# Optimization experiments

Hardware: AMD Instinct MI355X
Metric: run time of the kernel (lower is better)

Reference implementation:

```python
import jax, jax.numpy as jnp
import numpy as np

FILTER_SIZE = (9, 9)
N_ITER = 5  # training-mode iteration count (module forces 5 in train, 10 in eval)
DN = ('NCHW', 'OIHW', 'NCHW')


def _gauss_kernel1d(inv_theta, spacing, fsize):
    half = fsize // 2
    d = spacing * jnp.arange(-half, half + 1, dtype=jnp.float32)
    k = jnp.exp(-(d * inv_theta) ** 2 / 2)
    # zero out the center tap (message passing excludes self)
    return k * (jnp.arange(fsize) != half).astype(k.dtype)


def _blur_single(x, spacing, inv_theta):
    # x: (C, H, W); separable gaussian filtering with 'same' output via pre-padding
    ph, pw = FILTER_SIZE[0] // 2, FILTER_SIZE[1] // 2
    xp = jnp.pad(x, ((0, 0), (ph, ph), (pw, pw)))[:, None]  # (C, 1, H+2ph, W+2pw)
    kh = _gauss_kernel1d(inv_theta[0], spacing[0], FILTER_SIZE[0])
    kw = _gauss_kernel1d(inv_theta[1], spacing[1], FILTER_SIZE[1])
    xp = jax.lax.conv_general_dilated(xp, kh[None, None, :, None], (1, 1), 'VALID', dimension_numbers=DN)
    xp = jax.lax.conv_general_dilated(xp, kw[None, None, None, :], (1, 1), 'VALID', dimension_numbers=DN)
    return xp[:, 0]  # (C, H, W)


def setup_inputs() -> dict:
    key = jax.random.key(0)
    k1, _ = jax.random.split(key)
    B, H, W, C = 16, 384, 384, 21
    x = jax.random.normal(k1, (B, H, W, C), dtype=jnp.float32)
    spatial_spacings = jnp.ones((B, 2), dtype=jnp.float32)
    smoothness_weight = jnp.asarray(1.0, dtype=jnp.float32)
    inv_smoothness_theta = jnp.full((2,), 1.0 / 0.5, dtype=jnp.float32)  # 1/theta
    return {
        'x': x,
        'spatial_spacings': spatial_spacings,
        'smoothness_weight': smoothness_weight,
        'inv_smoothness_theta': inv_smoothness_theta,
    }


def reference(x, spatial_spacings, smoothness_weight, inv_smoothness_theta):
    xt = jnp.transpose(x, (0, 3, 1, 2))  # (B, C, H, W)
    negative_unary = xt
    C = xt.shape[1]
    # compatibility: -(l1 == l2) -> -I_C
    compat = -jnp.eye(C, dtype=xt.dtype)
    blur = jax.vmap(_blur_single, in_axes=(0, 0, None))

    def body(xc, _):
        p = jax.nn.softmax(xc, axis=1)
        s = smoothness_weight * blur(p, spatial_spacings, inv_smoothness_theta)
        c = jnp.einsum('bjhw,jk->bkhw', s, compat)
        return negative_unary - c, None

    xt, _ = jax.lax.scan(body, xt, None, length=N_ITER)
    # returns == 'logits'
    return jnp.transpose(xt, (0, 2, 3, 1))
```

## Files before the change

kernel.cpp:

```cpp
#include <hip/hip_runtime.h>
#include <hip/hip_fp16.h>


#define BB    16
#define Himg  384
#define Wimg  384
#define CC    21
#define TH    16
#define TW    16
#define RR    4
#define PH    (TH + 2*RR)
#define PW    (TW + 2*RR)
#define ROWF  (PW * CC)
#define NPIX  (PH * PW)
#define OUT_ELEMS (TH * TW * CC)
#define CHUNKS_ROW (ROWF / 4)
#define NCHUNK (PH * CHUNKS_ROW)
#define NTOT  (BB * Himg * Wimg * CC)

__global__ __launch_bounds__(256, 6)
void crf_iter_kernel(const float* __restrict__ xin,
                     const float* __restrict__ unary,
                     float* __restrict__ out,
                     const float* __restrict__ spacings,
                     const float* __restrict__ inv_theta,
                     const float* __restrict__ sw_ptr)
{
    __shared__ __align__(16) unsigned char smem[PH * ROWF * 2];
    __half* pbuf = (__half*)smem;

    const int tid = threadIdx.x;
    const int b   = blockIdx.z;
    const int h0  = blockIdx.y * TH;
    const int w0  = blockIdx.x * TW;

    const float sp_h = spacings[b * 2 + 0];
    const float sp_w = spacings[b * 2 + 1];
    const float ith  = inv_theta[0];
    const float itw  = inv_theta[1];
    const float sw   = sw_ptr[0];
    float kh[9], kw[9];
#pragma unroll
    for (int i = 0; i < 9; ++i) {
        float dh = sp_h * (float)(i - 4) * ith;
        float dw = sp_w * (float)(i - 4) * itw;
        kh[i] = (i == 4) ? 0.f : __expf(-0.5f * dh * dh);
        kw[i] = (i == 4) ? 0.f : __expf(-0.5f * dw * dw);
    }

    {
        uint2* pb8 = (uint2*)pbuf;
        for (int idx = tid; idx < NCHUNK; idx += 256) {
            int r  = idx / CHUNKS_ROW;
            int q  = idx - r * CHUNKS_ROW;
            int hh = h0 - RR + r;
            if (hh >= 0 && hh < Himg) {
                int basef = ((b * Himg + hh) * Wimg + (w0 - RR)) * CC + q * 4;
                int a = basef < 0 ? 0 : (basef > NTOT - 4 ? NTOT - 4 : basef);
                float4 v = *(const float4*)(xin + a);
                __half2 lo = __floats2half2_rn(v.x, v.y);
                __half2 hi = __floats2half2_rn(v.z, v.w);
                uint2 st;
                st.x = *(unsigned int*)&lo;
                st.y = *(unsigned int*)&hi;
                pb8[idx] = st;
            }
        }
    }
    __syncthreads();

    for (int p = tid; p < NPIX; p += 256) {
        int r   = p / PW;
        int cpx = p - r * PW;
        int hh  = h0 - RR + r;
        int gw  = w0 - RR + cpx;
        __half* px = pbuf + p * CC;
        if (hh >= 0 && hh < Himg && gw >= 0 && gw < Wimg) {
            float v[CC];
            float m = -1e30f;
#pragma unroll
            for (int c = 0; c < CC; ++c) { v[c] = __half2float(px[c]); m = fmaxf(m, v[c]); }
            float s = 0.f;
#pragma unroll
            for (int c = 0; c < CC; ++c) { v[c] = __expf(v[c] - m); s += v[c]; }
            float inv = 1.f / s;
#pragma unroll
            for (int c = 0; c < CC; ++c) px[c] = __float2half_rn(v[c] * inv);
        } else {
            const __half z = __float2half_rn(0.f);
#pragma unroll
            for (int c = 0; c < CC; ++c) px[c] = z;
        }
    }
    __syncthreads();

    if (tid < ROWF / 2) {
        __half2* pb2 = (__half2*)pbuf;
        const int o2 = tid;
        float2 v[PH];
#pragma unroll
        for (int r = 0; r < PH; ++r) v[r] = __half22float2(pb2[r * (ROWF / 2) + o2]);
#pragma unroll
        for (int t = 0; t < TH; ++t) {
            float ax = 0.f, ay = 0.f;
#pragma unroll
            for (int i = 0; i < 9; ++i) {
                if (i == 4) continue;
                ax = fmaf(kh[i], v[t + i].x, ax);
                ay = fmaf(kh[i], v[t + i].y, ay);
            }
            __half2 o; o.x = __float2half_rn(ax); o.y = __float2half_rn(ay);
            pb2[t * (ROWF / 2) + o2] = o;
        }
    }
    __syncthreads();

    for (int o = tid; o < TH * CC; o += 256) {
        int h = o / CC;
        int c = o - h * CC;
        __half* line = pbuf + h * ROWF + c;
        float v[PW];
#pragma unroll
        for (int wp = 0; wp < PW; ++wp) v[wp] = __half2float(line[wp * CC]);
#pragma unroll
        for (int wt = 0; wt < TW; ++wt) {
            float acc = 0.f;
#pragma unroll
            for (int j = 0; j < 9; ++j) {
                if (j == 4) continue;
                acc = fmaf(kw[j], v[wt + j], acc);
            }
            line[wt * CC] = __float2half_rn(sw * acc);
        }
    }
    __syncthreads();

    {
        const int gbase = ((b * Himg + h0) * Wimg + w0) * CC;
        for (int j = tid; j < OUT_ELEMS / 4; j += 256) {
            int hrow = j / (TW * CC / 4);
            int qq   = j - hrow * (TW * CC / 4);
            int g = gbase + hrow * (Wimg * CC) + qq * 4;
            float4 u = *(const float4*)(unary + g);
            const __half2* sh = (const __half2*)(pbuf + hrow * ROWF + qq * 4);
            float2 lo = __half22float2(sh[0]);
            float2 hi = __half22float2(sh[1]);
            float4 o;
            o.x = u.x + lo.x; o.y = u.y + lo.y;
            o.z = u.z + hi.x; o.w = u.w + hi.y;
            *(float4*)(out + g) = o;
        }
    }
}

extern "C" void kernel_launch(void* const* d_in, const int* in_sizes, int n_in,
                              void* d_out, int out_size, void* d_ws, size_t ws_size,
                              hipStream_t stream) {
    const float* x         = (const float*)d_in[0];
    const float* spacings  = (const float*)d_in[1];
    const float* sw        = (const float*)d_in[2];
    const float* inv_theta = (const float*)d_in[3];
    float* out = (float*)d_out;
    float* ws  = (float*)d_ws;

    dim3 grid(Wimg / TW, Himg / TH, BB);
    dim3 block(256);

    crf_iter_kernel<<<grid, block, 0, stream>>>(x,   x, out, spacings, inv_theta, sw);
    crf_iter_kernel<<<grid, block, 0, stream>>>(out, x, ws,  spacings, inv_theta, sw);
    crf_iter_kernel<<<grid, block, 0, stream>>>(ws,  x, out, spacings, inv_theta, sw);
    crf_iter_kernel<<<grid, block, 0, stream>>>(out, x, ws,  spacings, inv_theta, sw);
    crf_iter_kernel<<<grid, block, 0, stream>>>(ws,  x, out, spacings, inv_theta, sw);
}
```

Before: 991.9 us.

## Restructure CRF tile into channel-pair planes with packed fp16 symmetric blur

Changes the shared-memory layout from pixel-interleaved channels to 11 planes of half2 channel pairs. Softmax now reads each pixel directly from global memory. Both separable blur passes use packed fp16 adds and FMAs, exploiting the kernel's symmetry to halve the multiplies, and the smoothness weight is folded into the horizontal taps. The aim is to cut ALU work, fp32 conversions and bank conflicts in the blur. The cost is that global loads and stores become scalar strided per-pixel accesses instead of coalesced float4, and all blur arithmetic is done in fp16, which lowers accuracy.

```diff
diff --git a/kernel.cpp b/kernel.cpp
--- a/kernel.cpp
+++ b/kernel.cpp
@@ -6,17 +6,26 @@
 #define Himg  384
 #define Wimg  384
 #define CC    21
+#define NP    11
 #define TH    16
 #define TW    16
 #define RR    4
 #define PH    (TH + 2*RR)
 #define PW    (TW + 2*RR)
-#define ROWF  (PW * CC)
 #define NPIX  (PH * PW)
-#define OUT_ELEMS (TH * TW * CC)
-#define CHUNKS_ROW (ROWF / 4)
-#define NCHUNK (PH * CHUNKS_ROW)
-#define NTOT  (BB * Himg * Wimg * CC)
+#define PLANE_B 2384
+#define ROW_B   (PW * 4)
+#define NTASK (PW * NP)
+
+static __device__ __forceinline__ unsigned int pk_add(unsigned int a, unsigned int b) {
+    unsigned int d; asm("v_pk_add_f16 %0, %1, %2" : "=v"(d) : "v"(a), "v"(b)); return d;
+}
+static __device__ __forceinline__ unsigned int pk_mul(unsigned int a, unsigned int b) {
+    unsigned int d; asm("v_pk_mul_f16 %0, %1, %2" : "=v"(d) : "v"(a), "v"(b)); return d;
+}
+static __device__ __forceinline__ unsigned int pk_fma(unsigned int a, unsigned int b, unsigned int c) {
+    unsigned int d; asm("v_pk_fma_f16 %0, %1, %2, %3" : "=v"(d) : "v"(a), "v"(b), "v"(c)); return d;
+}
 
 __global__ __launch_bounds__(256, 6)
 void crf_iter_kernel(const float* __restrict__ xin,
@@ -26,8 +35,7 @@
                      const float* __restrict__ inv_theta,
                      const float* __restrict__ sw_ptr)
 {
-    __shared__ __align__(16) unsigned char smem[PH * ROWF * 2];
-    __half* pbuf = (__half*)smem;
+    __shared__ __align__(16) unsigned char smem[NP * PLANE_B];
 
     const int tid = threadIdx.x;
     const int b   = blockIdx.z;
@@ -39,117 +47,122 @@
     const float ith  = inv_theta[0];
     const float itw  = inv_theta[1];
     const float sw   = sw_ptr[0];
-    float kh[9], kw[9];
+    unsigned int khp[4], kwp[4];
 #pragma unroll
-    for (int i = 0; i < 9; ++i) {
+    for (int i = 0; i < 4; ++i) {
         float dh = sp_h * (float)(i - 4) * ith;
         float dw = sp_w * (float)(i - 4) * itw;
-        kh[i] = (i == 4) ? 0.f : __expf(-0.5f * dh * dh);
-        kw[i] = (i == 4) ? 0.f : __expf(-0.5f * dw * dw);
+        float kh = __expf(-0.5f * dh * dh);
+        float kw = sw * __expf(-0.5f * dw * dw);
+        __half2 a = __floats2half2_rn(kh, kh);
+        __half2 c = __floats2half2_rn(kw, kw);
+        khp[i] = *(unsigned int*)&a;
+        kwp[i] = *(unsigned int*)&c;
     }
 
-    {
-        uint2* pb8 = (uint2*)pbuf;
-        for (int idx = tid; idx < NCHUNK; idx += 256) {
-            int r  = idx / CHUNKS_ROW;
-            int q  = idx - r * CHUNKS_ROW;
-            int hh = h0 - RR + r;
-            if (hh >= 0 && hh < Himg) {
-                int basef = ((b * Himg + hh) * Wimg + (w0 - RR)) * CC + q * 4;
-                int a = basef < 0 ? 0 : (basef > NTOT - 4 ? NTOT - 4 : basef);
-                float4 v = *(const float4*)(xin + a);
-                __half2 lo = __floats2half2_rn(v.x, v.y);
-                __half2 hi = __floats2half2_rn(v.z, v.w);
-                uint2 st;
-                st.x = *(unsigned int*)&lo;
-                st.y = *(unsigned int*)&hi;
-                pb8[idx] = st;
+    for (int p = tid; p < NPIX; p += 256) {
+        const int r  = p / PW;
+        const int px = p - r * PW;
+        const int hh = h0 - RR + r;
+        const int gw = w0 - RR + px;
+        unsigned char* lbase = smem + p * 4;
+        if (hh >= 0 && hh < Himg && gw >= 0 && gw < Wimg) {
+            const float* gp = xin + ((b * Himg + hh) * Wimg + gw) * CC;
+            float v[CC];
+#pragma unroll
+            for (int c = 0; c < CC; ++c) v[c] = gp[c];
+            float m = v[0];
+#pragma unroll
+            for (int c = 1; c < CC; ++c) m = fmaxf(m, v[c]);
+            float s = 0.f;
+#pragma unroll
+            for (int c = 0; c < CC; ++c) { v[c] = __expf(v[c] - m); s += v[c]; }
+            const float inv = 1.0f / s;
+#pragma unroll
+            for (int cp = 0; cp < 10; ++cp) {
+                __half2 hx = __floats2half2_rn(v[2*cp] * inv, v[2*cp+1] * inv);
+                *(__half2*)(lbase + cp * PLANE_B) = hx;
             }
+            __half2 hl = __floats2half2_rn(v[20] * inv, 0.f);
+            *(__half2*)(lbase + 10 * PLANE_B) = hl;
+        } else {
+            const __half2 z = __floats2half2_rn(0.f, 0.f);
+#pragma unroll
+            for (int cp = 0; cp < NP; ++cp)
+                *(__half2*)(lbase + cp * PLANE_B) = z;
         }
     }
     __syncthreads();
 
-    for (int p = tid; p < NPIX; p += 256) {
-        int r   = p / PW;
-        int cpx = p - r * PW;
-        int hh  = h0 - RR + r;
-        int gw  = w0 - RR + cpx;
-        __half* px = pbuf + p * CC;
-        if (hh >= 0 && hh < Himg && gw >= 0 && gw < Wimg) {
-            float v[CC];
-            float m = -1e30f;
+    for (int t = tid; t < NTASK; t += 256) {
+        const int cp  = t / PW;
+        const int col = t - cp * PW;
+        unsigned char* base = smem + cp * PLANE_B + col * 4;
+        unsigned int v[PH];
 #pragma unroll
-            for (int c = 0; c < CC; ++c) { v[c] = __half2float(px[c]); m = fmaxf(m, v[c]); }
-            float s = 0.f;
+        for (int r = 0; r < PH; ++r) v[r] = *(const unsigned int*)(base + r * ROW_B);
 #pragma unroll
-            for (int c = 0; c < CC; ++c) { v[c] = __expf(v[c] - m); s += v[c]; }
-            float inv = 1.f / s;
-#pragma unroll
-            for (int c = 0; c < CC; ++c) px[c] = __float2half_rn(v[c] * inv);
-        } else {
-            const __half z = __float2half_rn(0.f);
-#pragma unroll
-            for (int c = 0; c < CC; ++c) px[c] = z;
+        for (int tt = 0; tt < TH; ++tt) {
+            unsigned int s0 = pk_add(v[tt],     v[tt + 8]);
+            unsigned int s1 = pk_add(v[tt + 1], v[tt + 7]);
+            unsigned int s2 = pk_add(v[tt + 2], v[tt + 6]);
+            unsigned int s3 = pk_add(v[tt + 3], v[tt + 5]);
+            unsigned int acc = pk_mul(khp[0], s0);
+            acc = pk_fma(khp[1], s1, acc);
+            acc = pk_fma(khp[2], s2, acc);
+            acc = pk_fma(khp[3], s3, acc);
+            *(unsigned int*)(base + tt * ROW_B) = acc;
         }
     }
     __syncthreads();
 
-    if (tid < ROWF / 2) {
-        __half2* pb2 = (__half2*)pbuf;
-        const int o2 = tid;
-        float2 v[PH];
+    if (tid < TH * NP) {
+        const int h  = tid / NP;
+        const int cp = tid - h * NP;
+        unsigned char* base = smem + cp * PLANE_B + h * ROW_B;
+        unsigned int v[PW];
 #pragma unroll
-        for (int r = 0; r < PH; ++r) v[r] = __half22float2(pb2[r * (ROWF / 2) + o2]);
-#pragma unroll
-        for (int t = 0; t < TH; ++t) {
-            float ax = 0.f, ay = 0.f;
-#pragma unroll
-            for (int i = 0; i < 9; ++i) {
-                if (i == 4) continue;
-                ax = fmaf(kh[i], v[t + i].x, ax);
-                ay = fmaf(kh[i], v[t + i].y, ay);
-            }
-            __half2 o; o.x = __float2half_rn(ax); o.y = __float2half_rn(ay);
-            pb2[t * (ROWF / 2) + o2] = o;
+        for (int k = 0; k < 6; ++k) {
+            const uint4 q = *(const uint4*)(base + k * 16);
+            v[4*k+0] = q.x; v[4*k+1] = q.y; v[4*k+2] = q.z; v[4*k+3] = q.w;
         }
-    }
-    __syncthreads();
-
-    for (int o = tid; o < TH * CC; o += 256) {
-        int h = o / CC;
-        int c = o - h * CC;
-        __half* line = pbuf + h * ROWF + c;
-        float v[PW];
-#pragma unroll
-        for (int wp = 0; wp < PW; ++wp) v[wp] = __half2float(line[wp * CC]);
+        unsigned int o[TW];
 #pragma unroll
         for (int wt = 0; wt < TW; ++wt) {
-            float acc = 0.f;
+            unsigned int s0 = pk_add(v[wt],     v[wt + 8]);
+            unsigned int s1 = pk_add(v[wt + 1], v[wt + 7]);
+            unsigned int s2 = pk_add(v[wt + 2], v[wt + 6]);
+            unsigned int s3 = pk_add(v[wt + 3], v[wt + 5]);
+            unsigned int acc = pk_mul(kwp[0], s0);
+            acc = pk_fma(kwp[1], s1, acc);
+            acc = pk_fma(kwp[2], s2, acc);
+            acc = pk_fma(kwp[3], s3, acc);
+            o[wt] = acc;
+        }
 #pragma unroll
-            for (int j = 0; j < 9; ++j) {
-                if (j == 4) continue;
-                acc = fmaf(kw[j], v[wt + j], acc);
-            }
-            line[wt * CC] = __float2half_rn(sw * acc);
+        for (int k = 0; k < 4; ++k) {
+            uint4 wq;
+            wq.x = o[4*k+0]; wq.y = o[4*k+1]; wq.z = o[4*k+2]; wq.w = o[4*k+3];
+            *(uint4*)(base + k * 16) = wq;
         }
     }
     __syncthreads();
 
     {
-        const int gbase = ((b * Himg + h0) * Wimg + w0) * CC;
-        for (int j = tid; j < OUT_ELEMS / 4; j += 256) {
-            int hrow = j / (TW * CC / 4);
-            int qq   = j - hrow * (TW * CC / 4);
-            int g = gbase + hrow * (Wimg * CC) + qq * 4;
-            float4 u = *(const float4*)(unary + g);
-            const __half2* sh = (const __half2*)(pbuf + hrow * ROWF + qq * 4);
-            float2 lo = __half22float2(sh[0]);
-            float2 hi = __half22float2(sh[1]);
-            float4 o;
-            o.x = u.x + lo.x; o.y = u.y + lo.y;
-            o.z = u.z + hi.x; o.w = u.w + hi.y;
-            *(float4*)(out + g) = o;
+        const int r  = tid >> 4;
+        const int px = tid & 15;
+        unsigned char* lbase = smem + (r * PW + px) * 4;
+        float sv[CC + 1];
+#pragma unroll
+        for (int cp = 0; cp < NP; ++cp) {
+            float2 f = __half22float2(*(const __half2*)(lbase + cp * PLANE_B));
+            sv[2*cp] = f.x; sv[2*cp+1] = f.y;
         }
+        const int g = ((b * Himg + h0 + r) * Wimg + (w0 + px)) * CC;
+        const float* up = unary + g;
+        float* op = out + g;
+#pragma unroll
+        for (int c = 0; c < CC; ++c) op[c] = up[c] + sv[c];
     }
 }
 
```

New measurement: 918.9 us. 1.08x faster.
